# Kernel tuning notes

Hardware: AMD Instinct MI355X
Metric: run time of the kernel (lower is better)

## Reference

```python
import jax, jax.numpy as jnp
import numpy as np

GRID_SHAPE = (32, 32)
TEMPERATURE = 1.0


def setup_inputs() -> dict:
    key = jax.random.key(0)
    k1, k2 = jax.random.split(key)
    x = jax.random.normal(k1, (16384, 1024), dtype=jnp.float32)
    som_weights = jax.random.normal(k2, (*GRID_SHAPE, 1024), dtype=jnp.float32) * 0.05
    return {"x": x, "som_weights": som_weights}


def reference(x, som_weights):
    # x: [B, D]; som_weights: [G1, G2, D]
    B, D = x.shape
    g1, g2 = GRID_SHAPE
    w_flat = som_weights.reshape(g1 * g2, D)  # [N, D]
    x_sq = jnp.sum(x * x, axis=-1, keepdims=True)          # [B, 1]
    w_sq = jnp.sum(w_flat * w_flat, axis=-1)[None, :]       # [1, N]
    d2 = x_sq - 2.0 * (x @ w_flat.T) + w_sq                 # [B, N]
    logits = (-d2 / TEMPERATURE).reshape(B, g1, g2)         # [B, G1, G2]
    # per-dimension softmax along each spatial axis, combined multiplicatively
    s1 = jax.nn.softmax(logits, axis=1)
    s2 = jax.nn.softmax(logits, axis=2)
    combined = s1 * s2
    combined = combined / (jnp.sum(combined, axis=(1, 2), keepdims=True) + 1e-8)
    # soft reconstruction: weighted sum over grid of codebook vectors
    recon = jnp.einsum('bn,nd->bd', combined.reshape(B, g1 * g2), w_flat)
    return recon
```

## Files before the change

### kernel.cpp

```cpp
#include <hip/hip_runtime.h>
#include <hip/hip_bf16.h>

static constexpr int BATCH = 16384;
static constexpr int DIM   = 1024;
static constexpr int NN    = 1024;
static constexpr int G     = 32;

typedef _Float16 half8  __attribute__((ext_vector_type(8)));
typedef _Float16 half4v __attribute__((ext_vector_type(4)));
typedef float    f32x4  __attribute__((ext_vector_type(4)));

__global__ __launch_bounds__(256) void cvt_x_kernel(const float* __restrict__ x,
                                                    _Float16* __restrict__ xh) {
    size_t i = ((size_t)blockIdx.x * 256 + threadIdx.x) * 8;
    f32x4 a = *(const f32x4*)(x + i);
    f32x4 b = *(const f32x4*)(x + i + 4);
    half8 h;
#pragma unroll
    for (int q = 0; q < 4; ++q) { h[q] = (_Float16)a[q]; h[4 + q] = (_Float16)b[q]; }
    *(half8*)(xh + i) = h;
}

__global__ __launch_bounds__(256) void transpose_w_kernel(const float* __restrict__ W,
                                                          _Float16* __restrict__ Wh,
                                                          _Float16* __restrict__ WTh) {
    __shared__ _Float16 tile[64][72];
    const int t  = threadIdx.x;
    const int n0 = (blockIdx.x & 15) * 64;
    const int d0 = (blockIdx.x >> 4) * 64;
#pragma unroll
    for (int p = 0; p < 4; ++p) {
        int n = n0 + p * 16 + (t >> 4);
        int d = d0 + (t & 15) * 4;
        float4 v = *(const float4*)(W + (size_t)n * DIM + d);
        half4v h;
        h[0] = (_Float16)v.x; h[1] = (_Float16)v.y;
        h[2] = (_Float16)v.z; h[3] = (_Float16)v.w;
        *(half4v*)(Wh + (size_t)n * DIM + d) = h;
#pragma unroll
        for (int k = 0; k < 4; ++k)
            tile[(t & 15) * 4 + k][p * 16 + (t >> 4)] = h[k];
    }
    __syncthreads();
#pragma unroll
    for (int p = 0; p < 4; ++p) {
        int dp = p * 16 + (t >> 4);
        int nc = (t & 15) * 4;
        half4v hv = *(const half4v*)&tile[dp][nc];
        *(half4v*)(WTh + (size_t)(d0 + dp) * NN + n0 + nc) = hv;
    }
}

__global__ __launch_bounds__(256) void wsq_kernel(const float* __restrict__ W,
                                                  float* __restrict__ wsq) {
    const int n = blockIdx.x;
    const int t = threadIdx.x;
    float4 v = *(const float4*)(W + (size_t)n * DIM + 4 * t);
    float ss = v.x * v.x + v.y * v.y + v.z * v.z + v.w * v.w;
#pragma unroll
    for (int o = 32; o > 0; o >>= 1) ss += __shfl_xor(ss, o, 64);
    __shared__ float red[4];
    if ((t & 63) == 0) red[t >> 6] = ss;
    __syncthreads();
    if (t == 0) wsq[n] = red[0] + red[1] + red[2] + red[3];
}

template <int EPI>
__global__ __launch_bounds__(256) void gemm_bt_kernel(const _Float16* __restrict__ A,
                                                      const _Float16* __restrict__ B,
                                                      float* __restrict__ C,
                                                      const float* __restrict__ wsq,
                                                      int M, int N, int K) {
    __shared__ __align__(16) _Float16 As[2][128 * 64];
    __shared__ __align__(16) _Float16 Bs[2][128 * 64];

    const int t  = threadIdx.x;
    const int l  = t & 63;
    const int wv = t >> 6;

    const int NT  = N >> 7;
    const int MT  = M >> 7;
    const int lid = blockIdx.x;
    const int xcd = lid & 7;
    const int i0  = lid >> 3;
    const int bn  = (i0 % NT) * 128;
    const int bm  = (xcd * (MT >> 3) + i0 / NT) * 128;

    const int wm = (wv >> 1) * 64;
    const int wn = (wv & 1) * 64;

    auto stage = [&](int buf, int k0) {
#pragma unroll
        for (int j = 0; j < 4; ++j) {
            int rbase = wv * 32 + j * 8;
            int row   = rbase + (l >> 3);
            int c     = (l & 7) ^ (row & 7);
            const _Float16* gA = A + (size_t)(bm + row) * K + k0 + c * 8;
            __builtin_amdgcn_global_load_lds(
                (const __attribute__((address_space(1))) void*)gA,
                (__attribute__((address_space(3))) void*)(&As[buf][rbase * 64]),
                16, 0, 0);
            const _Float16* gB = B + (size_t)(bn + row) * K + k0 + c * 8;
            __builtin_amdgcn_global_load_lds(
                (const __attribute__((address_space(1))) void*)gB,
                (__attribute__((address_space(3))) void*)(&Bs[buf][rbase * 64]),
                16, 0, 0);
        }
    };

    f32x4 acc[4][4] = {};
    stage(0, 0);
    __syncthreads();

    int cur = 0;
    for (int kt = 0; kt < K; kt += 64) {
        if (kt + 64 < K) stage(cur ^ 1, kt + 64);
#pragma unroll
        for (int sub = 0; sub < 2; ++sub) {
            half8 af[4], bf[4];
#pragma unroll
            for (int mi = 0; mi < 4; ++mi) {
                const _Float16* pa = &As[cur][(wm + (l & 15) + mi * 16) * 64];
                int c = sub * 4 + (l >> 4);
                af[mi] = *(const half8*)(pa + (c ^ (l & 7)) * 8);
            }
#pragma unroll
            for (int ni = 0; ni < 4; ++ni) {
                const _Float16* pb = &Bs[cur][(wn + (l & 15) + ni * 16) * 64];
                int c = sub * 4 + (l >> 4);
                bf[ni] = *(const half8*)(pb + (c ^ (l & 7)) * 8);
            }
#pragma unroll
            for (int mi = 0; mi < 4; ++mi)
#pragma unroll
                for (int ni = 0; ni < 4; ++ni)
                    acc[mi][ni] = __builtin_amdgcn_mfma_f32_16x16x32_f16(
                        af[mi], bf[ni], acc[mi][ni], 0, 0, 0);
        }
        __syncthreads();
        cur ^= 1;
    }

#pragma unroll
    for (int mi = 0; mi < 4; ++mi) {
        const int rbase = bm + wm + mi * 16 + (l >> 4) * 4;
#pragma unroll
        for (int ni = 0; ni < 4; ++ni) {
            const int col = bn + wn + ni * 16 + (l & 15);
            float wq = (EPI == 1) ? wsq[col] : 0.f;
#pragma unroll
            for (int r = 0; r < 4; ++r) {
                float v = acc[mi][ni][r];
                if (EPI == 1) v = 2.f * v - wq;
                C[(size_t)(rbase + r) * N + col] = v;
            }
        }
    }
}

__global__ __launch_bounds__(256) void softmax_kernel(const float* __restrict__ L,
                                                      _Float16* __restrict__ Ch) {
    const int l  = threadIdx.x & 63;
    const int wv = threadIdx.x >> 6;
    const int b  = blockIdx.x * 4 + wv;

    const f32x4* Lr = (const f32x4*)(L + (size_t)b * NN);
    f32x4 v[4];
#pragma unroll
    for (int i = 0; i < 4; ++i) v[i] = Lr[i * 64 + l];

    float er[4][4], ec[4][4];
    float rinv[4];
#pragma unroll
    for (int i = 0; i < 4; ++i) {
        float m = fmaxf(fmaxf(v[i][0], v[i][1]), fmaxf(v[i][2], v[i][3]));
        m = fmaxf(m, __shfl_xor(m, 1, 64));
        m = fmaxf(m, __shfl_xor(m, 2, 64));
        m = fmaxf(m, __shfl_xor(m, 4, 64));
        float s = 0.f;
#pragma unroll
        for (int j = 0; j < 4; ++j) { er[i][j] = __expf(v[i][j] - m); s += er[i][j]; }
        s += __shfl_xor(s, 1, 64);
        s += __shfl_xor(s, 2, 64);
        s += __shfl_xor(s, 4, 64);
        rinv[i] = 1.f / s;
    }
#pragma unroll
    for (int j = 0; j < 4; ++j) {
        float m = fmaxf(fmaxf(v[0][j], v[1][j]), fmaxf(v[2][j], v[3][j]));
        m = fmaxf(m, __shfl_xor(m, 8, 64));
        m = fmaxf(m, __shfl_xor(m, 16, 64));
        m = fmaxf(m, __shfl_xor(m, 32, 64));
        float s = 0.f;
#pragma unroll
        for (int i = 0; i < 4; ++i) { ec[i][j] = __expf(v[i][j] - m); s += ec[i][j]; }
        s += __shfl_xor(s, 8, 64);
        s += __shfl_xor(s, 16, 64);
        s += __shfl_xor(s, 32, 64);
        float ci = 1.f / s;
#pragma unroll
        for (int i = 0; i < 4; ++i) ec[i][j] *= ci;
    }
    float c[4][4];
    float tot = 0.f;
#pragma unroll
    for (int i = 0; i < 4; ++i)
#pragma unroll
        for (int j = 0; j < 4; ++j) {
            c[i][j] = er[i][j] * rinv[i] * ec[i][j];
            tot += c[i][j];
        }
#pragma unroll
    for (int o = 32; o > 0; o >>= 1) tot += __shfl_xor(tot, o, 64);
    float inv = 1.f / (tot + 1e-8f);
#pragma unroll
    for (int i = 0; i < 4; ++i) {
        half4v h;
#pragma unroll
        for (int j = 0; j < 4; ++j) h[j] = (_Float16)(c[i][j] * inv);
        ((half4v*)(Ch + (size_t)b * NN))[i * 64 + l] = h;
    }
}

extern "C" void kernel_launch(void* const* d_in, const int* in_sizes, int n_in,
                              void* d_out, int out_size, void* d_ws, size_t ws_size,
                              hipStream_t stream) {
    const float* x = (const float*)d_in[0];
    const float* w = (const float*)d_in[1];
    float* out = (float*)d_out;

    char* ws = (char*)d_ws;
    size_t off = 0;
    _Float16* ch  = (_Float16*)(ws + off); off += (size_t)BATCH * NN * 2;
    float*    L   = (float*)   (ws + off); off += (size_t)BATCH * NN * 4;
    _Float16* wh  = (_Float16*)(ws + off); off += (size_t)NN * DIM * 2;
    _Float16* wth = (_Float16*)(ws + off); off += (size_t)DIM * NN * 2;
    float*    wsq = (float*)   (ws + off); off += (size_t)NN * 4;

    _Float16* xh = ch;

    cvt_x_kernel<<<(BATCH * DIM) / (256 * 8), 256, 0, stream>>>(x, xh);
    transpose_w_kernel<<<256, 256, 0, stream>>>(w, wh, wth);
    wsq_kernel<<<NN, 256, 0, stream>>>(w, wsq);
    gemm_bt_kernel<1><<<(BATCH / 128) * (NN / 128), 256, 0, stream>>>(
        xh, wh, L, wsq, BATCH, NN, DIM);
    softmax_kernel<<<BATCH / 4, 256, 0, stream>>>(L, ch);
    gemm_bt_kernel<0><<<(BATCH / 128) * (DIM / 128), 256, 0, stream>>>(
        ch, wth, out, nullptr, BATCH, DIM, NN);
}
```

Baseline: 229.1 us.

## Fuse distance GEMM, dual softmax and reconstruction GEMM into one kernel

Replaces the two GEMM kernels and the separate softmax kernel with one fused kernel per 64-row block. Weights are pre-packed into MFMA fragment order and read straight from global/L2. Logits stay in registers, and the per-axis softmaxes are done in log-space with shuffles plus LDS cross-wave reductions. The fp16 combined weights are kept in LDS for the second GEMM, which removes the large fp32 logits and fp16 weight round trips through HBM. The cost is heavy LDS use (about 150KB) and high register pressure, with only 256 blocks of 512 threads, and the weight operand is reloaded from global by every block.

```diff
diff --git a/kernel.cpp b/kernel.cpp
--- a/kernel.cpp
+++ b/kernel.cpp
@@ -4,11 +4,12 @@
 static constexpr int BATCH = 16384;
 static constexpr int DIM   = 1024;
 static constexpr int NN    = 1024;
-static constexpr int G     = 32;
 
 typedef _Float16 half8  __attribute__((ext_vector_type(8)));
 typedef _Float16 half4v __attribute__((ext_vector_type(4)));
 typedef float    f32x4  __attribute__((ext_vector_type(4)));
+
+static constexpr float L2E = 1.44269504088896340736f;
 
 __global__ __launch_bounds__(256) void cvt_x_kernel(const float* __restrict__ x,
                                                     _Float16* __restrict__ xh) {
@@ -21,33 +22,31 @@
     *(half8*)(xh + i) = h;
 }
 
-__global__ __launch_bounds__(256) void transpose_w_kernel(const float* __restrict__ W,
-                                                          _Float16* __restrict__ Wh,
-                                                          _Float16* __restrict__ WTh) {
-    __shared__ _Float16 tile[64][72];
-    const int t  = threadIdx.x;
-    const int n0 = (blockIdx.x & 15) * 64;
-    const int d0 = (blockIdx.x >> 4) * 64;
-#pragma unroll
-    for (int p = 0; p < 4; ++p) {
-        int n = n0 + p * 16 + (t >> 4);
-        int d = d0 + (t & 15) * 4;
-        float4 v = *(const float4*)(W + (size_t)n * DIM + d);
-        half4v h;
-        h[0] = (_Float16)v.x; h[1] = (_Float16)v.y;
-        h[2] = (_Float16)v.z; h[3] = (_Float16)v.w;
-        *(half4v*)(Wh + (size_t)n * DIM + d) = h;
-#pragma unroll
-        for (int k = 0; k < 4; ++k)
-            tile[(t & 15) * 4 + k][p * 16 + (t >> 4)] = h[k];
-    }
-    __syncthreads();
-#pragma unroll
-    for (int p = 0; p < 4; ++p) {
-        int dp = p * 16 + (t >> 4);
-        int nc = (t & 15) * 4;
-        half4v hv = *(const half4v*)&tile[dp][nc];
-        *(half4v*)(WTh + (size_t)(d0 + dp) * NN + n0 + nc) = hv;
+__global__ __launch_bounds__(256) void prep_pack_kernel(const float* __restrict__ W,
+                                                        _Float16* __restrict__ P1,
+                                                        _Float16* __restrict__ P2) {
+    const int l = threadIdx.x & 63;
+    const int v = threadIdx.x >> 6;
+    const int f = blockIdx.x * 4 + v;
+    const int hi = f >> 5, lo = f & 31;
+    {
+        int n  = hi * 16 + (l & 15);
+        int k0 = lo * 32 + (l >> 4) * 8;
+        const float* src = W + (size_t)n * DIM + k0;
+        f32x4 a = *(const f32x4*)src;
+        f32x4 b = *(const f32x4*)(src + 4);
+        half8 h;
+#pragma unroll
+        for (int q = 0; q < 4; ++q) { h[q] = (_Float16)a[q]; h[4 + q] = (_Float16)b[q]; }
+        *(half8*)(P1 + ((size_t)f * 64 + l) * 8) = h;
+    }
+    {
+        int d  = hi * 16 + (l & 15);
+        int n0 = lo * 32 + (l >> 4) * 8;
+        half8 h;
+#pragma unroll
+        for (int j = 0; j < 8; ++j) h[j] = (_Float16)W[(size_t)(n0 + j) * DIM + d];
+        *(half8*)(P2 + ((size_t)f * 64 + l) * 8) = h;
     }
 }
 
@@ -65,160 +64,261 @@
     if (t == 0) wsq[n] = red[0] + red[1] + red[2] + red[3];
 }
 
-template <int EPI>
-__global__ __launch_bounds__(256) void gemm_bt_kernel(const _Float16* __restrict__ A,
-                                                      const _Float16* __restrict__ B,
-                                                      float* __restrict__ C,
-                                                      const float* __restrict__ wsq,
-                                                      int M, int N, int K) {
-    __shared__ __align__(16) _Float16 As[2][128 * 64];
-    __shared__ __align__(16) _Float16 Bs[2][128 * 64];
+__global__ __launch_bounds__(512, 2) void fused_som_kernel(
+    const _Float16* __restrict__ Xh, const _Float16* __restrict__ P1,
+    const _Float16* __restrict__ P2, const float* __restrict__ wsq,
+    float* __restrict__ Out) {
+
+    __shared__ __align__(16) _Float16 xs[2][64 * 64];
+    __shared__ __align__(16) char     BIG[131072];
+    __shared__ __align__(16) float    a1_lds[64 * 32];
 
     const int t  = threadIdx.x;
     const int l  = t & 63;
-    const int wv = t >> 6;
-
-    const int NT  = N >> 7;
-    const int MT  = M >> 7;
-    const int lid = blockIdx.x;
-    const int xcd = lid & 7;
-    const int i0  = lid >> 3;
-    const int bn  = (i0 % NT) * 128;
-    const int bm  = (xcd * (MT >> 3) + i0 / NT) * 128;
-
-    const int wm = (wv >> 1) * 64;
-    const int wn = (wv & 1) * 64;
-
-    auto stage = [&](int buf, int k0) {
-#pragma unroll
-        for (int j = 0; j < 4; ++j) {
-            int rbase = wv * 32 + j * 8;
-            int row   = rbase + (l >> 3);
-            int c     = (l & 7) ^ (row & 7);
-            const _Float16* gA = A + (size_t)(bm + row) * K + k0 + c * 8;
-            __builtin_amdgcn_global_load_lds(
-                (const __attribute__((address_space(1))) void*)gA,
-                (__attribute__((address_space(3))) void*)(&As[buf][rbase * 64]),
-                16, 0, 0);
-            const _Float16* gB = B + (size_t)(bn + row) * K + k0 + c * 8;
-            __builtin_amdgcn_global_load_lds(
-                (const __attribute__((address_space(1))) void*)gB,
-                (__attribute__((address_space(3))) void*)(&Bs[buf][rbase * 64]),
-                16, 0, 0);
-        }
+    const int w  = t >> 6;
+    const int r0 = blockIdx.x * 64;
+
+    auto stageA = [&](int buf, int kt) {
+        int row = t >> 3;
+        int c   = (t & 7) ^ (row & 7);
+        const _Float16* g = Xh + (size_t)(r0 + row) * DIM + kt + c * 8;
+        __builtin_amdgcn_global_load_lds(
+            (const __attribute__((address_space(1))) void*)g,
+            (__attribute__((address_space(3))) void*)(&xs[buf][(w * 8) * 64]),
+            16, 0, 0);
     };
 
-    f32x4 acc[4][4] = {};
-    stage(0, 0);
-    __syncthreads();
-
-    int cur = 0;
-    for (int kt = 0; kt < K; kt += 64) {
-        if (kt + 64 < K) stage(cur ^ 1, kt + 64);
-#pragma unroll
-        for (int sub = 0; sub < 2; ++sub) {
-            half8 af[4], bf[4];
-#pragma unroll
-            for (int mi = 0; mi < 4; ++mi) {
-                const _Float16* pa = &As[cur][(wm + (l & 15) + mi * 16) * 64];
-                int c = sub * 4 + (l >> 4);
-                af[mi] = *(const half8*)(pa + (c ^ (l & 7)) * 8);
-            }
-#pragma unroll
-            for (int ni = 0; ni < 4; ++ni) {
-                const _Float16* pb = &Bs[cur][(wn + (l & 15) + ni * 16) * 64];
-                int c = sub * 4 + (l >> 4);
-                bf[ni] = *(const half8*)(pb + (c ^ (l & 7)) * 8);
-            }
-#pragma unroll
-            for (int mi = 0; mi < 4; ++mi)
-#pragma unroll
-                for (int ni = 0; ni < 4; ++ni)
-                    acc[mi][ni] = __builtin_amdgcn_mfma_f32_16x16x32_f16(
-                        af[mi], bf[ni], acc[mi][ni], 0, 0, 0);
-        }
+    f32x4 acc[4][8] = {};
+    stageA(0, 0);
+    __syncthreads();
+
+    for (int kt = 0; kt < DIM; kt += 64) {
+        const int cur = (kt >> 6) & 1;
+        const int tk0 = kt >> 5;
+        half8 bf0[8], bf1[8];
+#pragma unroll
+        for (int ni = 0; ni < 8; ++ni) {
+            const size_t fb = (size_t)(w * 8 + ni) * 32;
+            bf0[ni] = *(const half8*)(P1 + ((fb + tk0) * 64 + l) * 8);
+            bf1[ni] = *(const half8*)(P1 + ((fb + tk0 + 1) * 64 + l) * 8);
+        }
+        if (kt + 64 < DIM) stageA(cur ^ 1, kt + 64);
+        half8 af[4];
+#pragma unroll
+        for (int mi = 0; mi < 4; ++mi) {
+            const _Float16* pa = &xs[cur][((l & 15) + mi * 16) * 64];
+            af[mi] = *(const half8*)(pa + ((0 + (l >> 4)) ^ (l & 7)) * 8);
+        }
+#pragma unroll
+        for (int mi = 0; mi < 4; ++mi)
+#pragma unroll
+            for (int ni = 0; ni < 8; ++ni)
+                acc[mi][ni] = __builtin_amdgcn_mfma_f32_16x16x32_f16(
+                    af[mi], bf0[ni], acc[mi][ni], 0, 0, 0);
+#pragma unroll
+        for (int mi = 0; mi < 4; ++mi) {
+            const _Float16* pa = &xs[cur][((l & 15) + mi * 16) * 64];
+            af[mi] = *(const half8*)(pa + ((4 + (l >> 4)) ^ (l & 7)) * 8);
+        }
+#pragma unroll
+        for (int mi = 0; mi < 4; ++mi)
+#pragma unroll
+            for (int ni = 0; ni < 8; ++ni)
+                acc[mi][ni] = __builtin_amdgcn_mfma_f32_16x16x32_f16(
+                    af[mi], bf1[ni], acc[mi][ni], 0, 0, 0);
         __syncthreads();
-        cur ^= 1;
-    }
-
+    }
+
+    float wq[8];
+#pragma unroll
+    for (int ni = 0; ni < 8; ++ni) wq[ni] = wsq[w * 128 + ni * 16 + (l & 15)];
+#pragma unroll
+    for (int mi = 0; mi < 4; ++mi)
+#pragma unroll
+        for (int ni = 0; ni < 8; ++ni)
+#pragma unroll
+            for (int q = 0; q < 4; ++q)
+                acc[mi][ni][q] = 2.f * acc[mi][ni][q] - wq[ni];
+
+    float* red = (float*)BIG;
+
+    f32x4 a2v[4][4];
+#pragma unroll
+    for (int mi = 0; mi < 4; ++mi)
+#pragma unroll
+        for (int p = 0; p < 4; ++p) {
+            f32x4 mx;
+#pragma unroll
+            for (int q = 0; q < 4; ++q)
+                mx[q] = fmaxf(acc[mi][2 * p][q], acc[mi][2 * p + 1][q]);
+#pragma unroll
+            for (int q = 0; q < 4; ++q) {
+                float m = mx[q];
+                m = fmaxf(m, __shfl_xor(m, 1, 64));
+                m = fmaxf(m, __shfl_xor(m, 2, 64));
+                m = fmaxf(m, __shfl_xor(m, 4, 64));
+                m = fmaxf(m, __shfl_xor(m, 8, 64));
+                mx[q] = m;
+            }
+#pragma unroll
+            for (int q = 0; q < 4; ++q) {
+                float s = exp2f((acc[mi][2 * p][q] - mx[q]) * L2E) +
+                          exp2f((acc[mi][2 * p + 1][q] - mx[q]) * L2E);
+                s += __shfl_xor(s, 1, 64);
+                s += __shfl_xor(s, 2, 64);
+                s += __shfl_xor(s, 4, 64);
+                s += __shfl_xor(s, 8, 64);
+                a2v[mi][p][q] = mx[q] * L2E + log2f(s);
+            }
+        }
+
+#pragma unroll
+    for (int mi = 0; mi < 4; ++mi)
+#pragma unroll
+        for (int j = 0; j < 2; ++j)
+#pragma unroll
+            for (int q = 0; q < 4; ++q) {
+                float pm = fmaxf(fmaxf(acc[mi][j][q], acc[mi][2 + j][q]),
+                                 fmaxf(acc[mi][4 + j][q], acc[mi][6 + j][q]));
+                int row = mi * 16 + (l >> 4) * 4 + q;
+                red[(w * 64 + row) * 33 + j * 16 + (l & 15)] = pm;
+            }
+    __syncthreads();
+#pragma unroll
+    for (int i = 0; i < 4; ++i) {
+        int pr = t + i * 512;
+        int row = pr >> 5, g2 = pr & 31;
+        float m = red[row * 33 + g2];
+#pragma unroll
+        for (int wv = 1; wv < 8; ++wv)
+            m = fmaxf(m, red[(wv * 64 + row) * 33 + g2]);
+        a1_lds[row * 32 + g2] = m;
+    }
+    __syncthreads();
+#pragma unroll
+    for (int mi = 0; mi < 4; ++mi)
+#pragma unroll
+        for (int j = 0; j < 2; ++j)
+#pragma unroll
+            for (int q = 0; q < 4; ++q) {
+                int row = mi * 16 + (l >> 4) * 4 + q;
+                float m1 = a1_lds[row * 32 + j * 16 + (l & 15)];
+                float s = 0.f;
+#pragma unroll
+                for (int p = 0; p < 4; ++p)
+                    s += exp2f((acc[mi][2 * p + j][q] - m1) * L2E);
+                red[(w * 64 + row) * 33 + j * 16 + (l & 15)] = s;
+            }
+    __syncthreads();
+#pragma unroll
+    for (int i = 0; i < 4; ++i) {
+        int pr = t + i * 512;
+        int row = pr >> 5, g2 = pr & 31;
+        float s = 0.f;
+#pragma unroll
+        for (int wv = 0; wv < 8; ++wv)
+            s += red[(wv * 64 + row) * 33 + g2];
+        a1_lds[row * 32 + g2] = a1_lds[row * 32 + g2] * L2E + log2f(s);
+    }
+    __syncthreads();
+
+    float* rowred = (float*)BIG;
 #pragma unroll
     for (int mi = 0; mi < 4; ++mi) {
-        const int rbase = bm + wm + mi * 16 + (l >> 4) * 4;
-#pragma unroll
-        for (int ni = 0; ni < 4; ++ni) {
-            const int col = bn + wn + ni * 16 + (l & 15);
-            float wq = (EPI == 1) ? wsq[col] : 0.f;
-#pragma unroll
-            for (int r = 0; r < 4; ++r) {
-                float v = acc[mi][ni][r];
-                if (EPI == 1) v = 2.f * v - wq;
-                C[(size_t)(rbase + r) * N + col] = v;
-            }
-        }
-    }
-}
-
-__global__ __launch_bounds__(256) void softmax_kernel(const float* __restrict__ L,
-                                                      _Float16* __restrict__ Ch) {
-    const int l  = threadIdx.x & 63;
-    const int wv = threadIdx.x >> 6;
-    const int b  = blockIdx.x * 4 + wv;
-
-    const f32x4* Lr = (const f32x4*)(L + (size_t)b * NN);
-    f32x4 v[4];
-#pragma unroll
-    for (int i = 0; i < 4; ++i) v[i] = Lr[i * 64 + l];
-
-    float er[4][4], ec[4][4];
-    float rinv[4];
-#pragma unroll
-    for (int i = 0; i < 4; ++i) {
-        float m = fmaxf(fmaxf(v[i][0], v[i][1]), fmaxf(v[i][2], v[i][3]));
-        m = fmaxf(m, __shfl_xor(m, 1, 64));
-        m = fmaxf(m, __shfl_xor(m, 2, 64));
-        m = fmaxf(m, __shfl_xor(m, 4, 64));
-        float s = 0.f;
-#pragma unroll
-        for (int j = 0; j < 4; ++j) { er[i][j] = __expf(v[i][j] - m); s += er[i][j]; }
-        s += __shfl_xor(s, 1, 64);
-        s += __shfl_xor(s, 2, 64);
-        s += __shfl_xor(s, 4, 64);
-        rinv[i] = 1.f / s;
-    }
-#pragma unroll
-    for (int j = 0; j < 4; ++j) {
-        float m = fmaxf(fmaxf(v[0][j], v[1][j]), fmaxf(v[2][j], v[3][j]));
-        m = fmaxf(m, __shfl_xor(m, 8, 64));
-        m = fmaxf(m, __shfl_xor(m, 16, 64));
-        m = fmaxf(m, __shfl_xor(m, 32, 64));
-        float s = 0.f;
-#pragma unroll
-        for (int i = 0; i < 4; ++i) { ec[i][j] = __expf(v[i][j] - m); s += ec[i][j]; }
-        s += __shfl_xor(s, 8, 64);
-        s += __shfl_xor(s, 16, 64);
-        s += __shfl_xor(s, 32, 64);
-        float ci = 1.f / s;
-#pragma unroll
-        for (int i = 0; i < 4; ++i) ec[i][j] *= ci;
-    }
-    float c[4][4];
-    float tot = 0.f;
-#pragma unroll
-    for (int i = 0; i < 4; ++i)
-#pragma unroll
-        for (int j = 0; j < 4; ++j) {
-            c[i][j] = er[i][j] * rinv[i] * ec[i][j];
-            tot += c[i][j];
-        }
-#pragma unroll
-    for (int o = 32; o > 0; o >>= 1) tot += __shfl_xor(tot, o, 64);
-    float inv = 1.f / (tot + 1e-8f);
-#pragma unroll
-    for (int i = 0; i < 4; ++i) {
-        half4v h;
-#pragma unroll
-        for (int j = 0; j < 4; ++j) h[j] = (_Float16)(c[i][j] * inv);
-        ((half4v*)(Ch + (size_t)b * NN))[i * 64 + l] = h;
+        f32x4 rs = {0.f, 0.f, 0.f, 0.f};
+#pragma unroll
+        for (int j = 0; j < 2; ++j) {
+            f32x4 a1v;
+#pragma unroll
+            for (int q = 0; q < 4; ++q) {
+                int row = mi * 16 + (l >> 4) * 4 + q;
+                a1v[q] = a1_lds[row * 32 + j * 16 + (l & 15)];
+            }
+#pragma unroll
+            for (int p = 0; p < 4; ++p)
+#pragma unroll
+                for (int q = 0; q < 4; ++q) {
+                    float cu = exp2f(acc[mi][2 * p + j][q] * (2.f * L2E)
+                                     - a1v[q] - a2v[mi][p][q]);
+                    acc[mi][2 * p + j][q] = cu;
+                    rs[q] += cu;
+                }
+        }
+#pragma unroll
+        for (int q = 0; q < 4; ++q) {
+            float sv = rs[q];
+            sv += __shfl_xor(sv, 1, 64);
+            sv += __shfl_xor(sv, 2, 64);
+            sv += __shfl_xor(sv, 4, 64);
+            sv += __shfl_xor(sv, 8, 64);
+            if ((l & 15) == 0) rowred[w * 64 + mi * 16 + (l >> 4) * 4 + q] = sv;
+        }
+    }
+    __syncthreads();
+    float* rowinv = ((float*)BIG) + 512;
+    if (t < 64) {
+        float tot = 0.f;
+#pragma unroll
+        for (int wv = 0; wv < 8; ++wv) tot += rowred[wv * 64 + t];
+        rowinv[t] = 1.f / (tot + 1e-8f);
+    }
+    __syncthreads();
+    f32x4 invr[4];
+#pragma unroll
+    for (int mi = 0; mi < 4; ++mi)
+#pragma unroll
+        for (int q = 0; q < 4; ++q)
+            invr[mi][q] = rowinv[mi * 16 + (l >> 4) * 4 + q];
+    __syncthreads();
+
+    _Float16* cs = (_Float16*)BIG;
+#pragma unroll
+    for (int mi = 0; mi < 4; ++mi)
+#pragma unroll
+        for (int ni = 0; ni < 8; ++ni) {
+            int chunk = w * 16 + ni * 2 + ((l & 15) >> 3);
+#pragma unroll
+            for (int q = 0; q < 4; ++q) {
+                int row = mi * 16 + (l >> 4) * 4 + q;
+                cs[row * 1024 + (chunk ^ (row & 7)) * 8 + (l & 7)] =
+                    (_Float16)(acc[mi][ni][q] * invr[mi][q]);
+            }
+        }
+    __syncthreads();
+
+    f32x4 acc2[4][8] = {};
+#pragma unroll 2
+    for (int kt = 0; kt < NN; kt += 32) {
+        const int tn = kt >> 5;
+        half8 bf[8], af2[4];
+#pragma unroll
+        for (int ni = 0; ni < 8; ++ni)
+            bf[ni] = *(const half8*)(P2 +
+                (((size_t)(w * 8 + ni) * 32 + tn) * 64 + l) * 8);
+#pragma unroll
+        for (int mi = 0; mi < 4; ++mi) {
+            int row = (l & 15) + mi * 16;
+            int kc  = tn * 4 + (l >> 4);
+            af2[mi] = *(const half8*)(cs + row * 1024 + (kc ^ (row & 7)) * 8);
+        }
+#pragma unroll
+        for (int mi = 0; mi < 4; ++mi)
+#pragma unroll
+            for (int ni = 0; ni < 8; ++ni)
+                acc2[mi][ni] = __builtin_amdgcn_mfma_f32_16x16x32_f16(
+                    af2[mi], bf[ni], acc2[mi][ni], 0, 0, 0);
+    }
+
+#pragma unroll
+    for (int mi = 0; mi < 4; ++mi) {
+        const int rbase = r0 + mi * 16 + (l >> 4) * 4;
+#pragma unroll
+        for (int ni = 0; ni < 8; ++ni) {
+            const int col = w * 128 + ni * 16 + (l & 15);
+#pragma unroll
+            for (int q = 0; q < 4; ++q)
+                Out[(size_t)(rbase + q) * DIM + col] = acc2[mi][ni][q];
+        }
     }
 }
 
@@ -231,20 +331,13 @@
 
     char* ws = (char*)d_ws;
     size_t off = 0;
-    _Float16* ch  = (_Float16*)(ws + off); off += (size_t)BATCH * NN * 2;
-    float*    L   = (float*)   (ws + off); off += (size_t)BATCH * NN * 4;
-    _Float16* wh  = (_Float16*)(ws + off); off += (size_t)NN * DIM * 2;
-    _Float16* wth = (_Float16*)(ws + off); off += (size_t)DIM * NN * 2;
-    float*    wsq = (float*)   (ws + off); off += (size_t)NN * 4;
-
-    _Float16* xh = ch;
+    _Float16* xh    = (_Float16*)(ws + off); off += (size_t)BATCH * DIM * 2;
+    _Float16* pack1 = (_Float16*)(ws + off); off += (size_t)NN * DIM * 2;
+    _Float16* pack2 = (_Float16*)(ws + off); off += (size_t)DIM * NN * 2;
+    float*    wsq   = (float*)   (ws + off); off += (size_t)NN * 4;
 
     cvt_x_kernel<<<(BATCH * DIM) / (256 * 8), 256, 0, stream>>>(x, xh);
-    transpose_w_kernel<<<256, 256, 0, stream>>>(w, wh, wth);
+    prep_pack_kernel<<<512, 256, 0, stream>>>(w, pack1, pack2);
     wsq_kernel<<<NN, 256, 0, stream>>>(w, wsq);
-    gemm_bt_kernel<1><<<(BATCH / 128) * (NN / 128), 256, 0, stream>>>(
-        xh, wh, L, wsq, BATCH, NN, DIM);
-    softmax_kernel<<<BATCH / 4, 256, 0, stream>>>(L, ch);
-    gemm_bt_kernel<0><<<(BATCH / 128) * (DIM / 128), 256, 0, stream>>>(
-        ch, wth, out, nullptr, BATCH, DIM, NN);
-}
+    fused_som_kernel<<<BATCH / 64, 512, 0, stream>>>(xh, pack1, pack2, wsq, out);
+}
```

After: 227.4 us. Within noise of the previous version (-0.7%).
